# Kernel optimization log

Measured on AMD Instinct MI355X. Metric: run time of the kernel, lower is better.

Reference implementation:

```python
import jax, jax.numpy as jnp
from jax import lax
import numpy as np

N, I, H, B, T = 16, 128, 128, 32, 512  # n lstms, input_size, hidden_size, batch, seq_len


def setup_inputs() -> dict:
    key = jax.random.key(0)
    k0, k1, k2, k3, k4 = jax.random.split(key, 5)
    s = 1.0 / np.sqrt(H)  # PyTorch LSTM init scale U(-1/sqrt(H), 1/sqrt(H)); normal*s is fine numerically
    x = jax.random.normal(k0, (B, T, N * I), dtype=jnp.float32)
    W_ih = jax.random.normal(k1, (N, 4 * H, I), dtype=jnp.float32) * s
    W_hh = jax.random.normal(k2, (N, 4 * H, H), dtype=jnp.float32) * s
    b_ih = jax.random.normal(k3, (N, 4 * H), dtype=jnp.float32) * s
    b_hh = jax.random.normal(k4, (N, 4 * H), dtype=jnp.float32) * s
    return {"x": x, "W_ih": W_ih, "W_hh": W_hh, "b_ih": b_ih, "b_hh": b_hh}


def reference(x, W_ih, W_hh, b_ih, b_hh):
    """WideLSTM fused forward: N independent single-layer unidirectional LSTMs,
    hx=None (zero initial state), batch_first output [B, T, N*H], (h_n, c_n) [1, B, N*H].
    PyTorch gate order: i, f, g, o."""
    Bx, Tx, _ = x.shape
    n = W_ih.shape[0]
    h = W_hh.shape[-1]
    xs = x.reshape(Bx, Tx, n, -1).transpose(1, 0, 2, 3)  # [T, B, N, I]
    # Precompute input contribution + biases for all timesteps at once (one big GEMM)
    x_proj = jnp.einsum('tbni,ngi->tbng', xs, W_ih) + (b_ih + b_hh)  # [T, B, N, 4H]

    def step(carry, xp):
        hprev, cprev = carry
        z = xp + jnp.einsum('bnh,ngh->bng', hprev, W_hh)  # [B, N, 4H]
        i_g, f_g, g_g, o_g = jnp.split(z, 4, axis=-1)
        i_g = jax.nn.sigmoid(i_g)
        f_g = jax.nn.sigmoid(f_g)
        g_g = jnp.tanh(g_g)
        o_g = jax.nn.sigmoid(o_g)
        c = f_g * cprev + i_g * g_g
        hnew = o_g * jnp.tanh(c)
        return (hnew, c), hnew

    h0 = jnp.zeros((Bx, n, h), dtype=x.dtype)
    c0 = jnp.zeros((Bx, n, h), dtype=x.dtype)
    (h_n, c_n), hs = lax.scan(step, (h0, c0), x_proj)
    output = hs.transpose(1, 0, 2, 3).reshape(Bx, Tx, n * h)  # [B, T, N*H]
    h_n = h_n.reshape(1, Bx, n * h)  # [num_layers*num_dir=1, B, N*H]
    c_n = c_n.reshape(1, Bx, n * h)
    return output, h_n, c_n
```

## Files before the change

### kernel.cpp

```cpp
#include <hip/hip_runtime.h>

#define N_LSTM 16
#define ISZ 128
#define HSZ 128
#define BSZ 32
#define TSZ 512
#define G4H 512
#define XROW (N_LSTM * ISZ)
#define OROW (N_LSTM * HSZ)

typedef __attribute__((ext_vector_type(8))) short s16x8;
typedef __attribute__((ext_vector_type(4))) float f32x4;

static __device__ __forceinline__ unsigned short f2bf(float f) {
    unsigned int u = __builtin_bit_cast(unsigned int, f);
    u += 0x7fffu + ((u >> 16) & 1u);
    return (unsigned short)(u >> 16);
}

static __device__ __forceinline__ float fast_sigmoid(float x) {
    float e = __expf(-x);
    return __builtin_amdgcn_rcpf(1.0f + e);
}

static __device__ __forceinline__ float fast_tanh(float x) {
    x = fminf(fmaxf(x, -20.0f), 20.0f);
    float e = __expf(-2.0f * x);
    return (1.0f - e) * __builtin_amdgcn_rcpf(1.0f + e);
}

__global__ __launch_bounds__(512, 2) void widelstm_fused(
    const float* __restrict__ x, const float* __restrict__ Wih,
    const float* __restrict__ Whh, const float* __restrict__ bih,
    const float* __restrict__ bhh, float* __restrict__ out)
{
    __shared__ __align__(16) unsigned short xbuf[2][16][136];
    __shared__ __align__(16) unsigned short hbuf[2][16][136];

    const int tid = threadIdx.x;
    const int wv  = tid >> 6;
    const int ln  = tid & 63;
    const int lm  = ln & 15;
    const int lq  = ln >> 4;
    const int n    = blockIdx.x >> 1;
    const int half = blockIdx.x & 1;
    const int b0   = half * 16;

    s16x8 wih[4][4], whh[4][4];
    float bias[4];
    #pragma unroll
    for (int g = 0; g < 4; ++g) {
        const int col = g * 128 + wv * 16 + lm;
        bias[g] = bih[n * G4H + col] + bhh[n * G4H + col];
        #pragma unroll
        for (int kt = 0; kt < 4; ++kt) {
            const float* pi = Wih + ((size_t)n * G4H + col) * ISZ + kt * 32 + lq * 8;
            const float* ph = Whh + ((size_t)n * G4H + col) * HSZ + kt * 32 + lq * 8;
            s16x8 a, b;
            #pragma unroll
            for (int j = 0; j < 8; ++j) {
                a[j] = (short)f2bf(pi[j]);
                b[j] = (short)f2bf(ph[j]);
            }
            wih[g][kt] = a;
            whh[g][kt] = b;
        }
    }

    for (int i = tid; i < 2 * 16 * 136; i += 512)
        ((unsigned short*)hbuf)[i] = 0;

    const int sr = tid >> 5;
    const int sc = (tid & 31) * 4;
    const float* xrow = x + (size_t)(b0 + sr) * TSZ * XROW + n * ISZ + sc;

    float4 xr = *(const float4*)(xrow);

    float cprev[4] = {0.f, 0.f, 0.f, 0.f};
    float hlast[4] = {0.f, 0.f, 0.f, 0.f};

    const int ocol = n * HSZ + wv * 16 + lm;

    #pragma unroll 1
    for (int t = 0; t < TSZ; ++t) {
        const int buf = t & 1;
        unsigned int lo = (unsigned int)f2bf(xr.x) | ((unsigned int)f2bf(xr.y) << 16);
        unsigned int hi = (unsigned int)f2bf(xr.z) | ((unsigned int)f2bf(xr.w) << 16);
        *(uint2*)&xbuf[buf][sr][sc] = make_uint2(lo, hi);
        __syncthreads();
        if (t + 1 < TSZ)
            xr = *(const float4*)(xrow + (size_t)(t + 1) * XROW);

        s16x8 ax[4], ah[4];
        #pragma unroll
        for (int kt = 0; kt < 4; ++kt) {
            ax[kt] = *(const s16x8*)&xbuf[buf][lm][kt * 32 + lq * 8];
            ah[kt] = *(const s16x8*)&hbuf[buf][lm][kt * 32 + lq * 8];
        }

        f32x4 acc[4];
        #pragma unroll
        for (int g = 0; g < 4; ++g)
            acc[g] = (f32x4){bias[g], bias[g], bias[g], bias[g]};
        #pragma unroll
        for (int kt = 0; kt < 4; ++kt) {
            #pragma unroll
            for (int g = 0; g < 4; ++g) {
                acc[g] = __builtin_amdgcn_mfma_f32_16x16x32_bf16(ax[kt], wih[g][kt], acc[g], 0, 0, 0);
                acc[g] = __builtin_amdgcn_mfma_f32_16x16x32_bf16(ah[kt], whh[g][kt], acc[g], 0, 0, 0);
            }
        }

        float* orow = out + (size_t)t * OROW + ocol;
        #pragma unroll
        for (int r = 0; r < 4; ++r) {
            float iv = fast_sigmoid(acc[0][r]);
            float fv = fast_sigmoid(acc[1][r]);
            float gv = fast_tanh(acc[2][r]);
            float ov = fast_sigmoid(acc[3][r]);
            float c  = fv * cprev[r] + iv * gv;
            cprev[r] = c;
            float hv = ov * fast_tanh(c);
            hlast[r] = hv;
            const int row = lq * 4 + r;
            orow[(size_t)(b0 + row) * TSZ * OROW] = hv;
            hbuf[buf ^ 1][row][wv * 16 + lm] = f2bf(hv);
        }
    }

    const size_t hn_off = (size_t)BSZ * TSZ * OROW;
    const size_t cn_off = hn_off + (size_t)BSZ * OROW;
    #pragma unroll
    for (int r = 0; r < 4; ++r) {
        const int row = lq * 4 + r;
        const size_t idx = (size_t)(b0 + row) * OROW + ocol;
        out[hn_off + idx] = hlast[r];
        out[cn_off + idx] = cprev[r];
    }
}

extern "C" void kernel_launch(void* const* d_in, const int* in_sizes, int n_in,
                              void* d_out, int out_size, void* d_ws, size_t ws_size,
                              hipStream_t stream) {
    const float* x   = (const float*)d_in[0];
    const float* Wih = (const float*)d_in[1];
    const float* Whh = (const float*)d_in[2];
    const float* bih = (const float*)d_in[3];
    const float* bhh = (const float*)d_in[4];
    float* out = (float*)d_out;
    widelstm_fused<<<dim3(32), dim3(512), 0, stream>>>(x, Wih, Whh, bih, bhh, out);
}
```

Measured before the change: 848.6 us.

## Split input projection into a parallel GEMM kernel before the recurrence

Computes the input projection plus biases for every timestep in a separate, highly parallel bf16 MFMA GEMM kernel and writes it to workspace. The recurrent kernel then does only the hidden-state MFMAs each step and prefetches the precomputed projections two steps ahead. This takes half of the serial per-step MFMA work and the x staging and sync off the critical path. In exchange it adds a 256MB bf16 workspace write and read, a second launch, and extra rounding of the pre-activations. The old fused kernel is kept as a fallback when the workspace is too small.

```diff
diff --git a/kernel.cpp b/kernel.cpp
--- a/kernel.cpp
+++ b/kernel.cpp
@@ -18,6 +18,11 @@
     return (unsigned short)(u >> 16);
 }
 
+static __device__ __forceinline__ float bf2f(unsigned short s) {
+    unsigned int u = ((unsigned int)s) << 16;
+    return __builtin_bit_cast(float, u);
+}
+
 static __device__ __forceinline__ float fast_sigmoid(float x) {
     float e = __expf(-x);
     return __builtin_amdgcn_rcpf(1.0f + e);
@@ -29,12 +34,102 @@
     return (1.0f - e) * __builtin_amdgcn_rcpf(1.0f + e);
 }
 
-__global__ __launch_bounds__(512, 2) void widelstm_fused(
+__global__ __launch_bounds__(256, 2) void xproj_gemm(
     const float* __restrict__ x, const float* __restrict__ Wih,
-    const float* __restrict__ Whh, const float* __restrict__ bih,
-    const float* __restrict__ bhh, float* __restrict__ out)
+    const float* __restrict__ bih, const float* __restrict__ bhh,
+    unsigned short* __restrict__ ws)
 {
-    __shared__ __align__(16) unsigned short xbuf[2][16][136];
+    __shared__ __align__(16) unsigned short xs[128][136];
+
+    const int tid = threadIdx.x;
+    const int w  = tid >> 6;
+    const int ln = tid & 63;
+    const int lm = ln & 15;
+    const int lq = ln >> 4;
+    const int bx  = blockIdx.x;
+    const int nt  = bx & 3;
+    const int mtb = (bx >> 2) & 127;
+    const int n   = bx >> 9;
+    const int R0  = mtb * 128;
+
+    #pragma unroll 1
+    for (int i = 0; i < 16; ++i) {
+        int flat = tid + i * 256;
+        int row  = flat >> 5;
+        int c4   = (flat & 31) * 4;
+        int rw   = R0 + row;
+        int t = rw >> 5, b = rw & 31;
+        const float4 v = *(const float4*)(x + ((size_t)b * TSZ + t) * XROW + n * ISZ + c4);
+        unsigned int lo = (unsigned int)f2bf(v.x) | ((unsigned int)f2bf(v.y) << 16);
+        unsigned int hi = (unsigned int)f2bf(v.z) | ((unsigned int)f2bf(v.w) << 16);
+        *(uint2*)&xs[row][c4] = make_uint2(lo, hi);
+    }
+    __syncthreads();
+
+    #pragma unroll 1
+    for (int cg = 0; cg < 2; ++cg) {
+        const int C0 = nt * 128 + cg * 64;
+        s16x8 bfr[4][4];
+        float bs[4];
+        #pragma unroll
+        for (int ct = 0; ct < 4; ++ct) {
+            const int col = C0 + ct * 16 + lm;
+            bs[ct] = bih[n * G4H + col] + bhh[n * G4H + col];
+            #pragma unroll
+            for (int kt = 0; kt < 4; ++kt) {
+                const float* p = Wih + ((size_t)n * G4H + col) * ISZ + kt * 32 + lq * 8;
+                s16x8 f;
+                #pragma unroll
+                for (int j = 0; j < 8; ++j) f[j] = (short)f2bf(p[j]);
+                bfr[ct][kt] = f;
+            }
+        }
+        #pragma unroll 1
+        for (int mt = 0; mt < 2; ++mt) {
+            const int lr = w * 32 + mt * 16;
+            s16x8 a[4];
+            #pragma unroll
+            for (int kt = 0; kt < 4; ++kt)
+                a[kt] = *(const s16x8*)&xs[lr + lm][kt * 32 + lq * 8];
+            f32x4 acc[4];
+            #pragma unroll
+            for (int ct = 0; ct < 4; ++ct)
+                acc[ct] = (f32x4){bs[ct], bs[ct], bs[ct], bs[ct]};
+            #pragma unroll
+            for (int kt = 0; kt < 4; ++kt)
+                #pragma unroll
+                for (int ct = 0; ct < 4; ++ct)
+                    acc[ct] = __builtin_amdgcn_mfma_f32_16x16x32_bf16(a[kt], bfr[ct][kt], acc[ct], 0, 0, 0);
+            #pragma unroll
+            for (int ct = 0; ct < 4; ++ct)
+                #pragma unroll
+                for (int r = 0; r < 4; ++r) {
+                    int rw = R0 + lr + lq * 4 + r;
+                    size_t off = ((size_t)rw * N_LSTM + n) * G4H + C0 + ct * 16 + lm;
+                    ws[off] = f2bf(acc[ct][r]);
+                }
+        }
+    }
+}
+
+static __device__ __forceinline__ void load_px(const unsigned short* __restrict__ xp,
+                                               int t, int b0, int n, int wv, int lm, int lq,
+                                               float px[16])
+{
+    #pragma unroll
+    for (int r = 0; r < 4; ++r) {
+        const unsigned short* p = xp
+            + ((size_t)((t * BSZ + b0 + lq * 4 + r) * N_LSTM + n)) * G4H + wv * 16 + lm;
+        #pragma unroll
+        for (int g = 0; g < 4; ++g)
+            px[r * 4 + g] = bf2f(p[g * 128]);
+    }
+}
+
+__global__ __launch_bounds__(512, 2) void lstm_rec(
+    const unsigned short* __restrict__ xp, const float* __restrict__ Whh,
+    float* __restrict__ out)
+{
     __shared__ __align__(16) unsigned short hbuf[2][16][136];
 
     const int tid = threadIdx.x;
@@ -46,6 +141,113 @@
     const int half = blockIdx.x & 1;
     const int b0   = half * 16;
 
+    s16x8 whh[4][4];
+    #pragma unroll
+    for (int g = 0; g < 4; ++g) {
+        const int col = g * 128 + wv * 16 + lm;
+        #pragma unroll
+        for (int kt = 0; kt < 4; ++kt) {
+            const float* ph = Whh + ((size_t)n * G4H + col) * HSZ + kt * 32 + lq * 8;
+            s16x8 b;
+            #pragma unroll
+            for (int j = 0; j < 8; ++j) b[j] = (short)f2bf(ph[j]);
+            whh[g][kt] = b;
+        }
+    }
+
+    for (int i = tid; i < 2 * 16 * 136; i += 512)
+        ((unsigned short*)hbuf)[i] = 0;
+
+    float cprev[4] = {0.f, 0.f, 0.f, 0.f};
+    float hlast[4] = {0.f, 0.f, 0.f, 0.f};
+
+    const int ocol = n * HSZ + wv * 16 + lm;
+    size_t obase[4];
+    #pragma unroll
+    for (int r = 0; r < 4; ++r)
+        obase[r] = (size_t)(b0 + lq * 4 + r) * TSZ * OROW + ocol;
+
+    float pxc[16], pxn[16];
+    load_px(xp, 0, b0, n, wv, lm, lq, pxc);
+    load_px(xp, 1, b0, n, wv, lm, lq, pxn);
+
+    size_t toff = 0;
+
+    #pragma unroll 2
+    for (int t = 0; t < TSZ; ++t) {
+        const int buf = t & 1;
+        __syncthreads();
+
+        s16x8 ah[4];
+        #pragma unroll
+        for (int kt = 0; kt < 4; ++kt)
+            ah[kt] = *(const s16x8*)&hbuf[buf][lm][kt * 32 + lq * 8];
+
+        float pxf[16];
+        int t2 = (t + 2 < TSZ) ? t + 2 : TSZ - 1;
+        load_px(xp, t2, b0, n, wv, lm, lq, pxf);
+
+        f32x4 acc[4];
+        #pragma unroll
+        for (int g = 0; g < 4; ++g)
+            acc[g] = (f32x4){pxc[g], pxc[4 + g], pxc[8 + g], pxc[12 + g]};
+
+        #pragma unroll
+        for (int kt = 0; kt < 4; ++kt)
+            #pragma unroll
+            for (int g = 0; g < 4; ++g)
+                acc[g] = __builtin_amdgcn_mfma_f32_16x16x32_bf16(ah[kt], whh[g][kt], acc[g], 0, 0, 0);
+
+        float hv[4];
+        #pragma unroll
+        for (int r = 0; r < 4; ++r) {
+            float iv = fast_sigmoid(acc[0][r]);
+            float fv = fast_sigmoid(acc[1][r]);
+            float gv = fast_tanh(acc[2][r]);
+            float ov = fast_sigmoid(acc[3][r]);
+            float c  = fv * cprev[r] + iv * gv;
+            cprev[r] = c;
+            float h  = ov * fast_tanh(c);
+            hv[r] = h;
+            hlast[r] = h;
+            hbuf[buf ^ 1][lq * 4 + r][wv * 16 + lm] = f2bf(h);
+        }
+        #pragma unroll
+        for (int r = 0; r < 4; ++r)
+            out[toff + obase[r]] = hv[r];
+        toff += OROW;
+
+        #pragma unroll
+        for (int i = 0; i < 16; ++i) { pxc[i] = pxn[i]; pxn[i] = pxf[i]; }
+    }
+
+    const size_t hn_off = (size_t)BSZ * TSZ * OROW;
+    const size_t cn_off = hn_off + (size_t)BSZ * OROW;
+    #pragma unroll
+    for (int r = 0; r < 4; ++r) {
+        const size_t idx = (size_t)(b0 + lq * 4 + r) * OROW + ocol;
+        out[hn_off + idx] = hlast[r];
+        out[cn_off + idx] = cprev[r];
+    }
+}
+
+__global__ __launch_bounds__(512, 2) void widelstm_fused(
+    const float* __restrict__ x, const float* __restrict__ Wih,
+    const float* __restrict__ Whh, const float* __restrict__ bih,
+    const float* __restrict__ bhh, float* __restrict__ out)
+{
+    __shared__ __align__(16) unsigned short xbuf[2][16][136];
+    __shared__ __align__(16) unsigned short hbuf[2][16][136];
+
+    const int tid = threadIdx.x;
+    const int wv  = tid >> 6;
+    const int ln  = tid & 63;
+    const int lm  = ln & 15;
+    const int lq  = ln >> 4;
+    const int n    = blockIdx.x >> 1;
+    const int half = blockIdx.x & 1;
+    const int b0   = half * 16;
+
     s16x8 wih[4][4], whh[4][4];
     float bias[4];
     #pragma unroll
@@ -58,12 +260,8 @@
             const float* ph = Whh + ((size_t)n * G4H + col) * HSZ + kt * 32 + lq * 8;
             s16x8 a, b;
             #pragma unroll
-            for (int j = 0; j < 8; ++j) {
-                a[j] = (short)f2bf(pi[j]);
-                b[j] = (short)f2bf(ph[j]);
-            }
-            wih[g][kt] = a;
-            whh[g][kt] = b;
+            for (int j = 0; j < 8; ++j) { a[j] = (short)f2bf(pi[j]); b[j] = (short)f2bf(ph[j]); }
+            wih[g][kt] = a; whh[g][kt] = b;
         }
     }
 
@@ -73,12 +271,10 @@
     const int sr = tid >> 5;
     const int sc = (tid & 31) * 4;
     const float* xrow = x + (size_t)(b0 + sr) * TSZ * XROW + n * ISZ + sc;
-
     float4 xr = *(const float4*)(xrow);
 
     float cprev[4] = {0.f, 0.f, 0.f, 0.f};
     float hlast[4] = {0.f, 0.f, 0.f, 0.f};
-
     const int ocol = n * HSZ + wv * 16 + lm;
 
     #pragma unroll 1
@@ -88,8 +284,7 @@
         unsigned int hi = (unsigned int)f2bf(xr.z) | ((unsigned int)f2bf(xr.w) << 16);
         *(uint2*)&xbuf[buf][sr][sc] = make_uint2(lo, hi);
         __syncthreads();
-        if (t + 1 < TSZ)
-            xr = *(const float4*)(xrow + (size_t)(t + 1) * XROW);
+        if (t + 1 < TSZ) xr = *(const float4*)(xrow + (size_t)(t + 1) * XROW);
 
         s16x8 ax[4], ah[4];
         #pragma unroll
@@ -97,20 +292,16 @@
             ax[kt] = *(const s16x8*)&xbuf[buf][lm][kt * 32 + lq * 8];
             ah[kt] = *(const s16x8*)&hbuf[buf][lm][kt * 32 + lq * 8];
         }
-
         f32x4 acc[4];
         #pragma unroll
-        for (int g = 0; g < 4; ++g)
-            acc[g] = (f32x4){bias[g], bias[g], bias[g], bias[g]};
-        #pragma unroll
-        for (int kt = 0; kt < 4; ++kt) {
+        for (int g = 0; g < 4; ++g) acc[g] = (f32x4){bias[g], bias[g], bias[g], bias[g]};
+        #pragma unroll
+        for (int kt = 0; kt < 4; ++kt)
             #pragma unroll
             for (int g = 0; g < 4; ++g) {
                 acc[g] = __builtin_amdgcn_mfma_f32_16x16x32_bf16(ax[kt], wih[g][kt], acc[g], 0, 0, 0);
                 acc[g] = __builtin_amdgcn_mfma_f32_16x16x32_bf16(ah[kt], whh[g][kt], acc[g], 0, 0, 0);
             }
-        }
-
         float* orow = out + (size_t)t * OROW + ocol;
         #pragma unroll
         for (int r = 0; r < 4; ++r) {
@@ -120,11 +311,11 @@
             float ov = fast_sigmoid(acc[3][r]);
             float c  = fv * cprev[r] + iv * gv;
             cprev[r] = c;
-            float hv = ov * fast_tanh(c);
-            hlast[r] = hv;
+            float h  = ov * fast_tanh(c);
+            hlast[r] = h;
             const int row = lq * 4 + r;
-            orow[(size_t)(b0 + row) * TSZ * OROW] = hv;
-            hbuf[buf ^ 1][row][wv * 16 + lm] = f2bf(hv);
+            orow[(size_t)(b0 + row) * TSZ * OROW] = h;
+            hbuf[buf ^ 1][row][wv * 16 + lm] = f2bf(h);
         }
     }
 
@@ -148,5 +339,13 @@
     const float* bih = (const float*)d_in[3];
     const float* bhh = (const float*)d_in[4];
     float* out = (float*)d_out;
-    widelstm_fused<<<dim3(32), dim3(512), 0, stream>>>(x, Wih, Whh, bih, bhh, out);
-}
+
+    const size_t need_bf16 = (size_t)TSZ * BSZ * N_LSTM * G4H * 2;
+    if (ws_size >= need_bf16) {
+        unsigned short* xp = (unsigned short*)d_ws;
+        xproj_gemm<<<dim3(8192), dim3(256), 0, stream>>>(x, Wih, bih, bhh, xp);
+        lstm_rec<<<dim3(32), dim3(512), 0, stream>>>(xp, Whh, out);
+    } else {
+        widelstm_fused<<<dim3(32), dim3(512), 0, stream>>>(x, Wih, Whh, bih, bhh, out);
+    }
+}
```

Result: slower. 1.073 ms (+26.5%).
